# Kernel tuning notes

Hardware: AMD Instinct MI355X
Metric: run time of the kernel (lower is better)

The kernel has to match this reference:

```python
import jax, jax.numpy as jnp
import numpy as np

N = 50000      # nodes
E = 800000     # edges (before self-loops)
IN = 256       # in_channels
HID = 16       # hidden_channels per head
HEADS = 8
OUT = 64       # out_channels (classes)
NEG_SLOPE = 0.2  # PyG GATConv leaky_relu slope


def setup_inputs() -> dict:
    key = jax.random.key(0)
    ks = jax.random.split(key, 10)
    x = jax.random.normal(ks[0], (N, IN), jnp.float32)
    edge_index = jax.random.randint(ks[1], (2, E), 0, N, dtype=jnp.int32)
    g = lambda k, shape: jax.random.normal(k, shape, jnp.float32) * (1.0 / np.sqrt(shape[0]))
    W1 = g(ks[2], (IN, HEADS * HID))
    a_src1 = jax.random.normal(ks[3], (HEADS, HID), jnp.float32) * 0.1
    a_dst1 = jax.random.normal(ks[4], (HEADS, HID), jnp.float32) * 0.1
    b1 = jnp.zeros((HEADS * HID,), jnp.float32)
    W2 = g(ks[5], (HEADS * HID, OUT))
    a_src2 = jax.random.normal(ks[6], (1, OUT), jnp.float32) * 0.1
    a_dst2 = jax.random.normal(ks[7], (1, OUT), jnp.float32) * 0.1
    b2 = jnp.zeros((OUT,), jnp.float32)
    return {"x": x, "edge_index": edge_index, "W1": W1, "a_src1": a_src1,
            "a_dst1": a_dst1, "b1": b1, "W2": W2, "a_src2": a_src2,
            "a_dst2": a_dst2, "b2": b2}


def gat_conv(x, src, dst, W, a_s, a_d, b, heads, concat):
    # x: [n, f]; edges src->dst; attention softmax over incoming edges of dst
    n = x.shape[0]
    h = (x @ W).reshape(n, heads, -1)                 # [n, H, d]
    al_s = jnp.einsum('nhd,hd->nh', h, a_s)           # [n, H]
    al_d = jnp.einsum('nhd,hd->nh', h, a_d)
    e = jax.nn.leaky_relu(al_s[src] + al_d[dst], negative_slope=NEG_SLOPE)  # [E, H]
    m = jax.ops.segment_max(e, dst, num_segments=n)   # stable scatter-softmax
    ex = jnp.exp(e - m[dst])
    den = jax.ops.segment_sum(ex, dst, num_segments=n)
    alpha = ex / (den[dst] + 1e-16)                   # [E, H]
    out = jax.ops.segment_sum(h[src] * alpha[:, :, None], dst, num_segments=n)  # [n, H, d]
    out = out.reshape(n, -1) if concat else out.mean(axis=1)
    return out + b


def reference(x, edge_index, W1, a_src1, a_dst1, b1, W2, a_src2, a_dst2, b2):
    # inference mode: dropout disabled. PyG GATConv adds self-loops by default.
    n = x.shape[0]
    loop = jnp.arange(n, dtype=edge_index.dtype)
    ei = jnp.concatenate([edge_index, jnp.stack([loop, loop])], axis=1)
    src, dst = ei[0], ei[1]
    h = gat_conv(x, src, dst, W1, a_src1, a_dst1, b1, HEADS, True)
    h = jax.nn.elu(h)
    h = gat_conv(h, src, dst, W2, a_src2, a_dst2, b2, 1, False)
    return jax.nn.log_softmax(h, axis=1)
```

## Files before the change

kernel.cpp:

```cpp
#include <hip/hip_runtime.h>
#include <hip/hip_bf16.h>


typedef __attribute__((ext_vector_type(8))) short short8;
typedef __attribute__((ext_vector_type(4))) float f4;

#define NCHUNK 64
#define NRANGE 4
#define RSIZE 16384

__device__ __forceinline__ unsigned short f2bf(float f) {
  unsigned int u = __builtin_bit_cast(unsigned int, f);
  u += 0x7fffu + ((u >> 16) & 1u);
  return (unsigned short)(u >> 16);
}
__device__ __forceinline__ float bf2f(unsigned short h) {
  unsigned int u = ((unsigned int)h) << 16;
  return __builtin_bit_cast(float, u);
}

__global__ __launch_bounds__(512) void hist_kernel(const int* __restrict__ ei,
                                                   int* __restrict__ hist,
                                                   int E, int N, int ET, int CS) {
  __shared__ int lh[RSIZE];
  const int c = blockIdx.x & (NCHUNK - 1);
  const int r = blockIdx.x >> 6;
  const int base = r * RSIZE;
  for (int i = threadIdx.x; i < RSIZE; i += 512) lh[i] = 0;
  __syncthreads();
  const int e0 = c * CS, e1 = min(e0 + CS, ET);
  for (int e = e0 + threadIdx.x; e < e1; e += 512) {
    int d = (e < E) ? ei[E + e] : (e - E);
    unsigned dl = (unsigned)(d - base);
    if (dl < RSIZE) atomicAdd(&lh[dl], 1);
  }
  __syncthreads();
  for (int i = threadIdx.x; i < RSIZE; i += 512) {
    int d = base + i;
    if (d < N) hist[c * N + d] = lh[i];
  }
}

__global__ __launch_bounds__(256) void colscan_kernel(int* __restrict__ hist,
                                                      int* __restrict__ deg, int N) {
  int d = blockIdx.x * 256 + threadIdx.x;
  if (d >= N) return;
  int run = 0;
#pragma unroll 8
  for (int c = 0; c < NCHUNK; ++c) {
    int v = hist[c * N + d];
    hist[c * N + d] = run;
    run += v;
  }
  deg[d] = run;
}

__global__ __launch_bounds__(1024) void scan1_kernel(const int* __restrict__ deg,
                                                     int* __restrict__ rowptr,
                                                     int* __restrict__ bsum, int N) {
  __shared__ int wtot[16];
  const int lane = threadIdx.x & 63, wid = threadIdx.x >> 6;
  int i = blockIdx.x * 1024 + threadIdx.x;
  int v = (i < N) ? deg[i] : 0;
  int incl = v;
#pragma unroll
  for (int off = 1; off < 64; off <<= 1) {
    int t = __shfl_up(incl, off, 64);
    if (lane >= off) incl += t;
  }
  if (lane == 63) wtot[wid] = incl;
  __syncthreads();
  int woff = 0;
#pragma unroll
  for (int w = 0; w < 16; ++w) woff += (w < wid) ? wtot[w] : 0;
  if (i < N) rowptr[i] = woff + incl - v;
  if (threadIdx.x == 1023) bsum[blockIdx.x] = woff + incl;
}

__global__ __launch_bounds__(64) void scan2_kernel(int* __restrict__ bsum, int NB) {
  int lane = threadIdx.x;
  int v = (lane < NB) ? bsum[lane] : 0;
  int incl = v;
#pragma unroll
  for (int off = 1; off < 64; off <<= 1) {
    int t = __shfl_up(incl, off, 64);
    if (lane >= off) incl += t;
  }
  if (lane < NB) bsum[lane] = incl - v;
}

__global__ __launch_bounds__(256) void scan3_kernel(int* __restrict__ rowptr,
                                                    const int* __restrict__ bsum,
                                                    int N, int ET) {
  int i = blockIdx.x * 256 + threadIdx.x;
  if (i < N) rowptr[i] += bsum[i >> 10];
  if (i == N) rowptr[N] = ET;
}

__global__ __launch_bounds__(512) void scatter2_kernel(const int* __restrict__ ei,
                                                       const int* __restrict__ hist,
                                                       const int* __restrict__ rowptr,
                                                       int* __restrict__ csr_src,
                                                       int E, int N, int ET, int CS) {
  __shared__ int lh[RSIZE];
  const int c = blockIdx.x & (NCHUNK - 1);
  const int r = blockIdx.x >> 6;
  const int base = r * RSIZE;
  for (int i = threadIdx.x; i < RSIZE; i += 512) {
    int d = base + i;
    lh[i] = (d < N) ? (rowptr[d] + hist[c * N + d]) : 0;
  }
  __syncthreads();
  const int e0 = c * CS, e1 = min(e0 + CS, ET);
  for (int e = e0 + threadIdx.x; e < e1; e += 512) {
    int s, d;
    if (e < E) { s = ei[e]; d = ei[E + e]; }
    else       { s = e - E; d = s; }
    unsigned dl = (unsigned)(d - base);
    if (dl < RSIZE) {
      int slot = atomicAdd(&lh[dl], 1);
      csr_src[slot] = s;
    }
  }
}

__global__ __launch_bounds__(256) void convw_kernel(const float* __restrict__ W1,
                                                    const float* __restrict__ W2,
                                                    unsigned short* __restrict__ Wt1,
                                                    unsigned short* __restrict__ Wt2) {
  int i = blockIdx.x * blockDim.x + threadIdx.x;
  if (i < 128 * 256) {
    int n = i >> 8, k = i & 255;
    Wt1[i] = f2bf(W1[k * 128 + n]);
  } else {
    int j = i - 128 * 256;
    if (j < 64 * 128) {
      int n = j >> 7, k = j & 127;
      Wt2[j] = f2bf(W2[k * 64 + n]);
    }
  }
}

__global__ __launch_bounds__(256) void gemm1_mfma(const float* __restrict__ X,
                                                  const unsigned short* __restrict__ Wt,
                                                  unsigned short* __restrict__ H,
                                                  int M) {
  __shared__ unsigned short at[64 * 40];
  __shared__ unsigned short btc[128 * 40];
  const int t = threadIdx.x;
  const int r0 = blockIdx.x * 64;
  const int wv = t >> 6, ln = t & 63;
  const int ml = ln & 15, q = ln >> 4;
  const int rw = (wv & 1) * 32, cw = (wv >> 1) * 64;

  const int arow = t >> 2, aks = (t & 3) * 8;
  const int bn0 = t >> 2, bks = (t & 3) * 8;
  const bool rok = (r0 + arow) < M;
  const float* xp = X + (size_t)(r0 + arow) * 256 + aks;
  const unsigned short* wp0 = Wt + (size_t)bn0 * 256 + bks;
  const unsigned short* wp1 = Wt + (size_t)(bn0 + 64) * 256 + bks;

  f4 acc[2][4];
#pragma unroll
  for (int a = 0; a < 2; ++a)
#pragma unroll
    for (int b = 0; b < 4; ++b) acc[a][b] = (f4)0.f;

  const float4 z4 = make_float4(0.f, 0.f, 0.f, 0.f);
  float4 pa0 = rok ? *(const float4*)(xp) : z4;
  float4 pa1 = rok ? *(const float4*)(xp + 4) : z4;
  short8 pb0 = *(const short8*)(wp0);
  short8 pb1 = *(const short8*)(wp1);

  for (int s = 0; s < 8; ++s) {
    __syncthreads();
    short8 av;
    av[0] = (short)f2bf(pa0.x); av[1] = (short)f2bf(pa0.y);
    av[2] = (short)f2bf(pa0.z); av[3] = (short)f2bf(pa0.w);
    av[4] = (short)f2bf(pa1.x); av[5] = (short)f2bf(pa1.y);
    av[6] = (short)f2bf(pa1.z); av[7] = (short)f2bf(pa1.w);
    *(short8*)&at[arow * 40 + aks] = av;
    *(short8*)&btc[bn0 * 40 + bks] = pb0;
    *(short8*)&btc[(bn0 + 64) * 40 + bks] = pb1;
    if (s < 7) {
      pa0 = rok ? *(const float4*)(xp + (s + 1) * 32) : z4;
      pa1 = rok ? *(const float4*)(xp + (s + 1) * 32 + 4) : z4;
      pb0 = *(const short8*)(wp0 + (s + 1) * 32);
      pb1 = *(const short8*)(wp1 + (s + 1) * 32);
    }
    __syncthreads();
    short8 af[2], bfr[4];
#pragma unroll
    for (int a = 0; a < 2; ++a)
      af[a] = *(const short8*)&at[(rw + a * 16 + ml) * 40 + q * 8];
#pragma unroll
    for (int b = 0; b < 4; ++b)
      bfr[b] = *(const short8*)&btc[(cw + b * 16 + ml) * 40 + q * 8];
#pragma unroll
    for (int a = 0; a < 2; ++a)
#pragma unroll
      for (int b = 0; b < 4; ++b)
        acc[a][b] = __builtin_amdgcn_mfma_f32_16x16x32_bf16(af[a], bfr[b], acc[a][b], 0, 0, 0);
  }

#pragma unroll
  for (int a = 0; a < 2; ++a)
#pragma unroll
    for (int i = 0; i < 4; ++i) {
      int rr = r0 + rw + a * 16 + q * 4 + i;
      if (rr < M) {
#pragma unroll
        for (int b = 0; b < 4; ++b)
          H[(size_t)rr * 128 + cw + b * 16 + ml] = f2bf(acc[a][b][i]);
      }
    }
}

__global__ __launch_bounds__(256) void gemm2_mfma(const unsigned short* __restrict__ Xb,
                                                  const unsigned short* __restrict__ Wt,
                                                  unsigned short* __restrict__ H,
                                                  int M) {
  __shared__ unsigned short at[64 * 40];
  __shared__ unsigned short btc[64 * 40];
  const int t = threadIdx.x;
  const int r0 = blockIdx.x * 64;
  const int wv = t >> 6, ln = t & 63;
  const int ml = ln & 15, q = ln >> 4;
  const int rw = (wv & 1) * 32, cw = (wv >> 1) * 32;

  const int arow = t >> 2, aks = (t & 3) * 8;
  const int bn = t >> 2, bks = (t & 3) * 8;
  const bool rok = (r0 + arow) < M;
  const unsigned short* xp = Xb + (size_t)(r0 + arow) * 128 + aks;
  const unsigned short* wp = Wt + (size_t)bn * 128 + bks;

  f4 acc[2][2];
#pragma unroll
  for (int a = 0; a < 2; ++a)
#pragma unroll
    for (int b = 0; b < 2; ++b) acc[a][b] = (f4)0.f;

  short8 pa = rok ? *(const short8*)(xp) : (short8)0;
  short8 pb = *(const short8*)(wp);

  for (int s = 0; s < 4; ++s) {
    __syncthreads();
    *(short8*)&at[arow * 40 + aks] = pa;
    *(short8*)&btc[bn * 40 + bks] = pb;
    if (s < 3) {
      pa = rok ? *(const short8*)(xp + (s + 1) * 32) : (short8)0;
      pb = *(const short8*)(wp + (s + 1) * 32);
    }
    __syncthreads();
    short8 af[2], bfr[2];
#pragma unroll
    for (int a = 0; a < 2; ++a)
      af[a] = *(const short8*)&at[(rw + a * 16 + ml) * 40 + q * 8];
#pragma unroll
    for (int b = 0; b < 2; ++b)
      bfr[b] = *(const short8*)&btc[(cw + b * 16 + ml) * 40 + q * 8];
#pragma unroll
    for (int a = 0; a < 2; ++a)
#pragma unroll
      for (int b = 0; b < 2; ++b)
        acc[a][b] = __builtin_amdgcn_mfma_f32_16x16x32_bf16(af[a], bfr[b], acc[a][b], 0, 0, 0);
  }

#pragma unroll
  for (int a = 0; a < 2; ++a)
#pragma unroll
    for (int i = 0; i < 4; ++i) {
      int rr = r0 + rw + a * 16 + q * 4 + i;
      if (rr < M) {
#pragma unroll
        for (int b = 0; b < 2; ++b)
          H[(size_t)rr * 64 + cw + b * 16 + ml] = f2bf(acc[a][b][i]);
      }
    }
}

__global__ __launch_bounds__(256) void dots1_kernel(const unsigned short* __restrict__ h1,
                                                    const float* __restrict__ as,
                                                    const float* __restrict__ ad,
                                                    float* __restrict__ als,
                                                    float* __restrict__ ald, int N) {
  int wave = (blockIdx.x * blockDim.x + threadIdx.x) >> 6;
  int lane = threadIdx.x & 63;
  if (wave >= N) return;
  float x0 = bf2f(h1[(size_t)wave * 128 + lane]);
  float x1 = bf2f(h1[(size_t)wave * 128 + 64 + lane]);
  float s0 = x0 * as[lane], s1 = x1 * as[64 + lane];
  float d0 = x0 * ad[lane], d1 = x1 * ad[64 + lane];
#pragma unroll
  for (int off = 8; off; off >>= 1) {
    s0 += __shfl_down(s0, off, 16); s1 += __shfl_down(s1, off, 16);
    d0 += __shfl_down(d0, off, 16); d1 += __shfl_down(d1, off, 16);
  }
  if ((lane & 15) == 0) {
    int h = lane >> 4;
    als[wave * 8 + h] = s0; als[wave * 8 + 4 + h] = s1;
    ald[wave * 8 + h] = d0; ald[wave * 8 + 4 + h] = d1;
  }
}

__global__ __launch_bounds__(256) void dots2_kernel(const unsigned short* __restrict__ h2,
                                                    const float* __restrict__ as,
                                                    const float* __restrict__ ad,
                                                    float* __restrict__ als,
                                                    float* __restrict__ ald, int N) {
  int wave = (blockIdx.x * blockDim.x + threadIdx.x) >> 6;
  int lane = threadIdx.x & 63;
  if (wave >= N) return;
  float x = bf2f(h2[(size_t)wave * 64 + lane]);
  float s = x * as[lane], d = x * ad[lane];
#pragma unroll
  for (int off = 32; off; off >>= 1) {
    s += __shfl_xor(s, off, 64);
    d += __shfl_xor(d, off, 64);
  }
  if (lane == 0) { als[wave] = s; ald[wave] = d; }
}

__global__ __launch_bounds__(256) void attn1_kernel(
    const unsigned short* __restrict__ h1, const float* __restrict__ als,
    const float* __restrict__ ald, const float* __restrict__ b1,
    const int* __restrict__ rowptr, const int* __restrict__ csr_src,
    unsigned short* __restrict__ helu, int N) {
  int d = __builtin_amdgcn_readfirstlane(
      (blockIdx.x * blockDim.x + threadIdx.x) >> 6);
  int lane = threadIdx.x & 63;
  if (d >= N) return;
  const int h = lane >> 3;
  const float aldd = ald[d * 8 + h];
  const int beg = rowptr[d], end = rowptr[d + 1];
  float den = 0.f;
  float ax = 0.f, ay = 0.f;
  int p = beg;
  for (; p + 4 <= end; p += 4) {
    int s0 = csr_src[p + 0], s1 = csr_src[p + 1];
    int s2 = csr_src[p + 2], s3 = csr_src[p + 3];
    float v0 = als[s0 * 8 + h] + aldd; v0 = v0 > 0.f ? v0 : 0.2f * v0;
    float v1 = als[s1 * 8 + h] + aldd; v1 = v1 > 0.f ? v1 : 0.2f * v1;
    float v2 = als[s2 * 8 + h] + aldd; v2 = v2 > 0.f ? v2 : 0.2f * v2;
    float v3 = als[s3 * 8 + h] + aldd; v3 = v3 > 0.f ? v3 : 0.2f * v3;
    float w0 = __expf(v0), w1 = __expf(v1), w2 = __expf(v2), w3 = __expf(v3);
    ushort2 g0 = *(const ushort2*)(h1 + (size_t)s0 * 128 + 2 * lane);
    ushort2 g1 = *(const ushort2*)(h1 + (size_t)s1 * 128 + 2 * lane);
    ushort2 g2 = *(const ushort2*)(h1 + (size_t)s2 * 128 + 2 * lane);
    ushort2 g3 = *(const ushort2*)(h1 + (size_t)s3 * 128 + 2 * lane);
    den += (w0 + w1) + (w2 + w3);
    ax += w0 * bf2f(g0.x) + w1 * bf2f(g1.x) + w2 * bf2f(g2.x) + w3 * bf2f(g3.x);
    ay += w0 * bf2f(g0.y) + w1 * bf2f(g1.y) + w2 * bf2f(g2.y) + w3 * bf2f(g3.y);
  }
  for (; p < end; ++p) {
    int s = csr_src[p];
    float v = als[s * 8 + h] + aldd; v = v > 0.f ? v : 0.2f * v;
    float w = __expf(v);
    ushort2 g = *(const ushort2*)(h1 + (size_t)s * 128 + 2 * lane);
    den += w;
    ax += w * bf2f(g.x); ay += w * bf2f(g.y);
  }
  float inv = 1.0f / (den + 1e-16f);
  float2 bb = *(const float2*)(b1 + 2 * lane);
  float o0 = ax * inv + bb.x;
  float o1 = ay * inv + bb.y;
  o0 = o0 > 0.f ? o0 : __expf(o0) - 1.0f;
  o1 = o1 > 0.f ? o1 : __expf(o1) - 1.0f;
  ushort2 ov; ov.x = f2bf(o0); ov.y = f2bf(o1);
  *(ushort2*)(helu + (size_t)d * 128 + 2 * lane) = ov;
}

__global__ __launch_bounds__(256) void attn2_kernel(
    const unsigned short* __restrict__ h2, const float* __restrict__ als,
    const float* __restrict__ ald, const float* __restrict__ b2,
    const int* __restrict__ rowptr, const int* __restrict__ csr_src,
    float* __restrict__ out, int N) {
  int d = __builtin_amdgcn_readfirstlane(
      (blockIdx.x * blockDim.x + threadIdx.x) >> 6);
  int lane = threadIdx.x & 63;
  if (d >= N) return;
  const float aldd = ald[d];
  const int beg = rowptr[d], end = rowptr[d + 1];
  float den = 0.f, acc = 0.f;
  int p = beg;
  for (; p + 4 <= end; p += 4) {
    int s0 = csr_src[p + 0], s1 = csr_src[p + 1];
    int s2 = csr_src[p + 2], s3 = csr_src[p + 3];
    float v0 = als[s0] + aldd; v0 = v0 > 0.f ? v0 : 0.2f * v0;
    float v1 = als[s1] + aldd; v1 = v1 > 0.f ? v1 : 0.2f * v1;
    float v2 = als[s2] + aldd; v2 = v2 > 0.f ? v2 : 0.2f * v2;
    float v3 = als[s3] + aldd; v3 = v3 > 0.f ? v3 : 0.2f * v3;
    float w0 = __expf(v0), w1 = __expf(v1), w2 = __expf(v2), w3 = __expf(v3);
    float g0 = bf2f(h2[(size_t)s0 * 64 + lane]);
    float g1 = bf2f(h2[(size_t)s1 * 64 + lane]);
    float g2 = bf2f(h2[(size_t)s2 * 64 + lane]);
    float g3 = bf2f(h2[(size_t)s3 * 64 + lane]);
    den += (w0 + w1) + (w2 + w3);
    acc += w0 * g0 + w1 * g1 + w2 * g2 + w3 * g3;
  }
  for (; p < end; ++p) {
    int s = csr_src[p];
    float v = als[s] + aldd; v = v > 0.f ? v : 0.2f * v;
    float w = __expf(v);
    den += w;
    acc += w * bf2f(h2[(size_t)s * 64 + lane]);
  }
  float z = acc / (den + 1e-16f) + b2[lane];
  float zm = z;
#pragma unroll
  for (int off = 32; off; off >>= 1) zm = fmaxf(zm, __shfl_xor(zm, off, 64));
  float ex = __expf(z - zm), se = ex;
#pragma unroll
  for (int off = 32; off; off >>= 1) se += __shfl_xor(se, off, 64);
  out[(size_t)d * 64 + lane] = z - zm - __logf(se);
}

extern "C" void kernel_launch(void* const* d_in, const int* in_sizes, int n_in,
                              void* d_out, int out_size, void* d_ws, size_t ws_size,
                              hipStream_t stream) {
  const int N = in_sizes[0] / 256;
  const int E = in_sizes[1] / 2;
  const int ET = E + N;
  const int CS = (ET + NCHUNK - 1) / NCHUNK;
  const int NB = (N + 1023) / 1024;

  const float* x   = (const float*)d_in[0];
  const int*   ei  = (const int*)d_in[1];
  const float* W1  = (const float*)d_in[2];
  const float* as1 = (const float*)d_in[3];
  const float* ad1 = (const float*)d_in[4];
  const float* b1  = (const float*)d_in[5];
  const float* W2  = (const float*)d_in[6];
  const float* as2 = (const float*)d_in[7];
  const float* ad2 = (const float*)d_in[8];
  const float* b2  = (const float*)d_in[9];
  float* out = (float*)d_out;

  char* p = (char*)d_ws;
  unsigned short* h1b  = (unsigned short*)p; p += (size_t)N * 128 * 2;
  unsigned short* h2b  = h1b;
  unsigned short* helu = (unsigned short*)p; p += (size_t)NCHUNK * N * 4;
  int* hist = (int*)helu;
  unsigned short* Wt1  = (unsigned short*)p; p += (size_t)128 * 256 * 2;
  unsigned short* Wt2  = (unsigned short*)p; p += (size_t)64 * 128 * 2;
  float* als1 = (float*)p; p += (size_t)N * 8 * 4;
  float* ald1 = (float*)p; p += (size_t)N * 8 * 4;
  float* als2 = (float*)p; p += (size_t)N * 4;
  float* ald2 = (float*)p; p += (size_t)N * 4;
  int* deg     = (int*)p; p += (size_t)N * 4;
  int* rowptr  = (int*)p; p += (size_t)(N + 1) * 4;
  int* bsum    = (int*)p; p += 64 * 4;
  int* csr_src = (int*)p; p += (size_t)ET * 4;

  convw_kernel<<<(128 * 256 + 64 * 128 + 255) / 256, 256, 0, stream>>>(W1, W2, Wt1, Wt2);

  hist_kernel<<<NCHUNK * NRANGE, 512, 0, stream>>>(ei, hist, E, N, ET, CS);
  colscan_kernel<<<(N + 255) / 256, 256, 0, stream>>>(hist, deg, N);
  scan1_kernel<<<NB, 1024, 0, stream>>>(deg, rowptr, bsum, N);
  scan2_kernel<<<1, 64, 0, stream>>>(bsum, NB);
  scan3_kernel<<<(N + 256) / 256, 256, 0, stream>>>(rowptr, bsum, N, ET);
  scatter2_kernel<<<NCHUNK * NRANGE, 512, 0, stream>>>(ei, hist, rowptr, csr_src, E, N, ET, CS);

  gemm1_mfma<<<(N + 63) / 64, 256, 0, stream>>>(x, Wt1, h1b, N);
  dots1_kernel<<<(N + 3) / 4, 256, 0, stream>>>(h1b, as1, ad1, als1, ald1, N);
  attn1_kernel<<<(N + 3) / 4, 256, 0, stream>>>(h1b, als1, ald1, b1, rowptr, csr_src, helu, N);

  gemm2_mfma<<<(N + 63) / 64, 256, 0, stream>>>(helu, Wt2, h2b, N);
  dots2_kernel<<<(N + 3) / 4, 256, 0, stream>>>(h2b, as2, ad2, als2, ald2, N);
  attn2_kernel<<<(N + 3) / 4, 256, 0, stream>>>(h2b, als2, ald2, b2, rowptr, csr_src, out, N);
}
```

Baseline: 290.6 us.

## Replace LDS-staged GEMMs with direct-register MFMA loading per wave

Both node-feature GEMMs drop shared-memory staging and block-wide barriers. Each wave now handles 16 rows and all output columns, loads its A fragments straight from global memory into registers, and reads the small bf16 weight fragments directly from global memory, relying on cache hits. This removes the LDS traffic and __syncthreads that the old version paid per K step. In exchange, weights are reloaded by every wave instead of shared within a block, and register pressure rises because a full row slice of X (16 float4s per lane in gemm1) is held at once.

```diff
diff --git a/kernel.cpp b/kernel.cpp
--- a/kernel.cpp
+++ b/kernel.cpp
@@ -141,142 +141,98 @@
   }
 }
 
-__global__ __launch_bounds__(256) void gemm1_mfma(const float* __restrict__ X,
-                                                  const unsigned short* __restrict__ Wt,
-                                                  unsigned short* __restrict__ H,
-                                                  int M) {
-  __shared__ unsigned short at[64 * 40];
-  __shared__ unsigned short btc[128 * 40];
+__global__ __launch_bounds__(256) void gemm1_direct(const float* __restrict__ X,
+                                                    const unsigned short* __restrict__ Wt,
+                                                    unsigned short* __restrict__ H,
+                                                    int M) {
   const int t = threadIdx.x;
-  const int r0 = blockIdx.x * 64;
   const int wv = t >> 6, ln = t & 63;
   const int ml = ln & 15, q = ln >> 4;
-  const int rw = (wv & 1) * 32, cw = (wv >> 1) * 64;
-
-  const int arow = t >> 2, aks = (t & 3) * 8;
-  const int bn0 = t >> 2, bks = (t & 3) * 8;
-  const bool rok = (r0 + arow) < M;
-  const float* xp = X + (size_t)(r0 + arow) * 256 + aks;
-  const unsigned short* wp0 = Wt + (size_t)bn0 * 256 + bks;
-  const unsigned short* wp1 = Wt + (size_t)(bn0 + 64) * 256 + bks;
-
-  f4 acc[2][4];
-#pragma unroll
-  for (int a = 0; a < 2; ++a)
-#pragma unroll
-    for (int b = 0; b < 4; ++b) acc[a][b] = (f4)0.f;
-
-  const float4 z4 = make_float4(0.f, 0.f, 0.f, 0.f);
-  float4 pa0 = rok ? *(const float4*)(xp) : z4;
-  float4 pa1 = rok ? *(const float4*)(xp + 4) : z4;
-  short8 pb0 = *(const short8*)(wp0);
-  short8 pb1 = *(const short8*)(wp1);
-
+  const int r0 = blockIdx.x * 64 + wv * 16;
+  if (r0 >= M) return;
+  const int arow = min(r0 + ml, M - 1);
+  const float* xp = X + (size_t)arow * 256 + q * 8;
+
+  float4 a0[8], a1[8];
+#pragma unroll
   for (int s = 0; s < 8; ++s) {
-    __syncthreads();
+    a0[s] = *(const float4*)(xp + s * 32);
+    a1[s] = *(const float4*)(xp + s * 32 + 4);
+  }
+
+  f4 acc[8];
+#pragma unroll
+  for (int b = 0; b < 8; ++b) acc[b] = (f4)0.f;
+
+  const unsigned short* wp = Wt + (size_t)ml * 256 + q * 8;
+#pragma unroll
+  for (int s = 0; s < 8; ++s) {
+    short8 bfr[8];
+#pragma unroll
+    for (int b = 0; b < 8; ++b)
+      bfr[b] = *(const short8*)(wp + (size_t)b * 16 * 256 + s * 32);
     short8 av;
-    av[0] = (short)f2bf(pa0.x); av[1] = (short)f2bf(pa0.y);
-    av[2] = (short)f2bf(pa0.z); av[3] = (short)f2bf(pa0.w);
-    av[4] = (short)f2bf(pa1.x); av[5] = (short)f2bf(pa1.y);
-    av[6] = (short)f2bf(pa1.z); av[7] = (short)f2bf(pa1.w);
-    *(short8*)&at[arow * 40 + aks] = av;
-    *(short8*)&btc[bn0 * 40 + bks] = pb0;
-    *(short8*)&btc[(bn0 + 64) * 40 + bks] = pb1;
-    if (s < 7) {
-      pa0 = rok ? *(const float4*)(xp + (s + 1) * 32) : z4;
-      pa1 = rok ? *(const float4*)(xp + (s + 1) * 32 + 4) : z4;
-      pb0 = *(const short8*)(wp0 + (s + 1) * 32);
-      pb1 = *(const short8*)(wp1 + (s + 1) * 32);
+    av[0] = (short)f2bf(a0[s].x); av[1] = (short)f2bf(a0[s].y);
+    av[2] = (short)f2bf(a0[s].z); av[3] = (short)f2bf(a0[s].w);
+    av[4] = (short)f2bf(a1[s].x); av[5] = (short)f2bf(a1[s].y);
+    av[6] = (short)f2bf(a1[s].z); av[7] = (short)f2bf(a1[s].w);
+#pragma unroll
+    for (int b = 0; b < 8; ++b)
+      acc[b] = __builtin_amdgcn_mfma_f32_16x16x32_bf16(av, bfr[b], acc[b], 0, 0, 0);
+  }
+
+#pragma unroll
+  for (int i = 0; i < 4; ++i) {
+    int rr = r0 + q * 4 + i;
+    if (rr < M) {
+#pragma unroll
+      for (int b = 0; b < 8; ++b)
+        H[(size_t)rr * 128 + b * 16 + ml] = f2bf(acc[b][i]);
     }
-    __syncthreads();
-    short8 af[2], bfr[4];
-#pragma unroll
-    for (int a = 0; a < 2; ++a)
-      af[a] = *(const short8*)&at[(rw + a * 16 + ml) * 40 + q * 8];
-#pragma unroll
-    for (int b = 0; b < 4; ++b)
-      bfr[b] = *(const short8*)&btc[(cw + b * 16 + ml) * 40 + q * 8];
-#pragma unroll
-    for (int a = 0; a < 2; ++a)
-#pragma unroll
-      for (int b = 0; b < 4; ++b)
-        acc[a][b] = __builtin_amdgcn_mfma_f32_16x16x32_bf16(af[a], bfr[b], acc[a][b], 0, 0, 0);
-  }
-
-#pragma unroll
-  for (int a = 0; a < 2; ++a)
-#pragma unroll
-    for (int i = 0; i < 4; ++i) {
-      int rr = r0 + rw + a * 16 + q * 4 + i;
-      if (rr < M) {
-#pragma unroll
-        for (int b = 0; b < 4; ++b)
-          H[(size_t)rr * 128 + cw + b * 16 + ml] = f2bf(acc[a][b][i]);
-      }
-    }
-}
-
-__global__ __launch_bounds__(256) void gemm2_mfma(const unsigned short* __restrict__ Xb,
-                                                  const unsigned short* __restrict__ Wt,
-                                                  unsigned short* __restrict__ H,
-                                                  int M) {
-  __shared__ unsigned short at[64 * 40];
-  __shared__ unsigned short btc[64 * 40];
+  }
+}
+
+__global__ __launch_bounds__(256) void gemm2_direct(const unsigned short* __restrict__ Xb,
+                                                    const unsigned short* __restrict__ Wt,
+                                                    unsigned short* __restrict__ H,
+                                                    int M) {
   const int t = threadIdx.x;
-  const int r0 = blockIdx.x * 64;
   const int wv = t >> 6, ln = t & 63;
   const int ml = ln & 15, q = ln >> 4;
-  const int rw = (wv & 1) * 32, cw = (wv >> 1) * 32;
-
-  const int arow = t >> 2, aks = (t & 3) * 8;
-  const int bn = t >> 2, bks = (t & 3) * 8;
-  const bool rok = (r0 + arow) < M;
-  const unsigned short* xp = Xb + (size_t)(r0 + arow) * 128 + aks;
-  const unsigned short* wp = Wt + (size_t)bn * 128 + bks;
-
-  f4 acc[2][2];
-#pragma unroll
-  for (int a = 0; a < 2; ++a)
-#pragma unroll
-    for (int b = 0; b < 2; ++b) acc[a][b] = (f4)0.f;
-
-  short8 pa = rok ? *(const short8*)(xp) : (short8)0;
-  short8 pb = *(const short8*)(wp);
-
+  const int r0 = blockIdx.x * 64 + wv * 16;
+  if (r0 >= M) return;
+  const int arow = min(r0 + ml, M - 1);
+  const unsigned short* xp = Xb + (size_t)arow * 128 + q * 8;
+
+  short8 av[4];
+#pragma unroll
+  for (int s = 0; s < 4; ++s) av[s] = *(const short8*)(xp + s * 32);
+
+  f4 acc[4];
+#pragma unroll
+  for (int b = 0; b < 4; ++b) acc[b] = (f4)0.f;
+
+  const unsigned short* wp = Wt + (size_t)ml * 128 + q * 8;
+#pragma unroll
   for (int s = 0; s < 4; ++s) {
-    __syncthreads();
-    *(short8*)&at[arow * 40 + aks] = pa;
-    *(short8*)&btc[bn * 40 + bks] = pb;
-    if (s < 3) {
-      pa = rok ? *(const short8*)(xp + (s + 1) * 32) : (short8)0;
-      pb = *(const short8*)(wp + (s + 1) * 32);
+    short8 bfr[4];
+#pragma unroll
+    for (int b = 0; b < 4; ++b)
+      bfr[b] = *(const short8*)(wp + (size_t)b * 16 * 128 + s * 32);
+#pragma unroll
+    for (int b = 0; b < 4; ++b)
+      acc[b] = __builtin_amdgcn_mfma_f32_16x16x32_bf16(av[s], bfr[b], acc[b], 0, 0, 0);
+  }
+
+#pragma unroll
+  for (int i = 0; i < 4; ++i) {
+    int rr = r0 + q * 4 + i;
+    if (rr < M) {
+#pragma unroll
+      for (int b = 0; b < 4; ++b)
+        H[(size_t)rr * 64 + b * 16 + ml] = f2bf(acc[b][i]);
     }
-    __syncthreads();
-    short8 af[2], bfr[2];
-#pragma unroll
-    for (int a = 0; a < 2; ++a)
-      af[a] = *(const short8*)&at[(rw + a * 16 + ml) * 40 + q * 8];
-#pragma unroll
-    for (int b = 0; b < 2; ++b)
-      bfr[b] = *(const short8*)&btc[(cw + b * 16 + ml) * 40 + q * 8];
-#pragma unroll
-    for (int a = 0; a < 2; ++a)
-#pragma unroll
-      for (int b = 0; b < 2; ++b)
-        acc[a][b] = __builtin_amdgcn_mfma_f32_16x16x32_bf16(af[a], bfr[b], acc[a][b], 0, 0, 0);
-  }
-
-#pragma unroll
-  for (int a = 0; a < 2; ++a)
-#pragma unroll
-    for (int i = 0; i < 4; ++i) {
-      int rr = r0 + rw + a * 16 + q * 4 + i;
-      if (rr < M) {
-#pragma unroll
-        for (int b = 0; b < 2; ++b)
-          H[(size_t)rr * 64 + cw + b * 16 + ml] = f2bf(acc[a][b][i]);
-      }
-    }
+  }
 }
 
 __global__ __launch_bounds__(256) void dots1_kernel(const unsigned short* __restrict__ h1,
@@ -461,11 +417,11 @@
   scan3_kernel<<<(N + 256) / 256, 256, 0, stream>>>(rowptr, bsum, N, ET);
   scatter2_kernel<<<NCHUNK * NRANGE, 512, 0, stream>>>(ei, hist, rowptr, csr_src, E, N, ET, CS);
 
-  gemm1_mfma<<<(N + 63) / 64, 256, 0, stream>>>(x, Wt1, h1b, N);
+  gemm1_direct<<<(N + 63) / 64, 256, 0, stream>>>(x, Wt1, h1b, N);
   dots1_kernel<<<(N + 3) / 4, 256, 0, stream>>>(h1b, as1, ad1, als1, ald1, N);
   attn1_kernel<<<(N + 3) / 4, 256, 0, stream>>>(h1b, als1, ald1, b1, rowptr, csr_src, helu, N);
 
-  gemm2_mfma<<<(N + 63) / 64, 256, 0, stream>>>(helu, Wt2, h2b, N);
+  gemm2_direct<<<(N + 63) / 64, 256, 0, stream>>>(helu, Wt2, h2b, N);
   dots2_kernel<<<(N + 3) / 4, 256, 0, stream>>>(h2b, as2, ad2, als2, ald2, N);
   attn2_kernel<<<(N + 3) / 4, 256, 0, stream>>>(h2b, als2, ald2, b2, rowptr, csr_src, out, N);
 }
```

Result: slower. 296.5 us (+2.0%).
